# Kernel optimization log

Measured on AMD Instinct MI355X. Metric: run time of the kernel, lower is better.

Reference implementation:

```python
import jax, jax.numpy as jnp
import numpy as np

K_SIZE = 7
D_MODEL = 128
D_Q = 64
N_HEADS = 4
D_FF = 512
EPS = 1e-5


def _windows(x, k):
    # x: [N,E,H,W] -> [N,E,P,H,W]; zero-padded local k x k windows,
    # row-major over (dy,dx), matching nn.Unfold ordering.
    p = k // 2
    N, E, H, W = x.shape
    xp = jnp.pad(x, ((0, 0), (0, 0), (p, p), (p, p)))
    ws = [xp[:, :, i:i + H, j:j + W] for i in range(k) for j in range(k)]
    return jnp.stack(ws, axis=2)


def _layernorm(x, g, b):
    m = jnp.mean(x, -1, keepdims=True)
    v = jnp.var(x, -1, keepdims=True)
    return (x - m) * jax.lax.rsqrt(v + EPS) * g + b


def setup_inputs() -> dict:
    key = jax.random.key(0)
    ks = jax.random.split(key, 12)
    E, Q, F = D_MODEL, D_Q, D_FF

    def g(k, shape, s=0.02):
        return jax.random.normal(k, shape, jnp.float32) * s

    return dict(
        x=jax.random.normal(ks[0], (4, E, 64, 64), jnp.float32),
        qcoeff=jax.random.normal(ks[1], (4, Q), jnp.float32),
        wq=g(ks[2], (E, E)), bq=jnp.zeros((E,), jnp.float32),
        wk=g(ks[3], (E, E)), bk=jnp.zeros((E,), jnp.float32),
        wv=g(ks[4], (E, E)), bv=jnp.zeros((E,), jnp.float32),
        rel_bias=jnp.zeros((N_HEADS, K_SIZE * K_SIZE), jnp.float32),
        ln1_g=jnp.ones((E,), jnp.float32), ln1_b=jnp.zeros((E,), jnp.float32),
        bil_w=g(ks[5], (E, E, Q)), bil_b=jnp.zeros((E,), jnp.float32),
        ln2_g=jnp.ones((E,), jnp.float32), ln2_b=jnp.zeros((E,), jnp.float32),
        w1=g(ks[6], (F, E)), b1=jnp.zeros((F,), jnp.float32),
        w2=g(ks[7], (E, F)), b2=jnp.zeros((E,), jnp.float32),
    )


def reference(x, qcoeff, wq, bq, wk, bk, wv, bv, rel_bias, ln1_g, ln1_b,
              bil_w, bil_b, ln2_g, ln2_b, w1, b1, w2, b2):
    N, E, H, W = x.shape
    Nh = N_HEADS
    Hd = E // Nh
    P = K_SIZE * K_SIZE

    x_nhwc = jnp.transpose(x, (0, 2, 3, 1))              # [N,H,W,E]
    xn = _layernorm(x_nhwc, ln1_g, ln1_b)
    xnc = jnp.transpose(xn, (0, 3, 1, 2))                # [N,E,H,W]

    # 1x1-conv projections
    q = jnp.einsum('nchw,oc->nohw', xnc, wq) + bq[None, :, None, None]
    k = jnp.einsum('nchw,oc->nohw', xnc, wk) + bk[None, :, None, None]
    v = jnp.einsum('nchw,oc->nohw', xnc, wv) + bv[None, :, None, None]

    # local windows of K/V: [N,Nh,Hd,P,H,W]
    Kw = _windows(k, K_SIZE).reshape(N, Nh, Hd, P, H, W)
    Vw = _windows(v, K_SIZE).reshape(N, Nh, Hd, P, H, W)
    Qh = q.reshape(N, Nh, Hd, H, W)

    scores = jnp.einsum('nhdyx,nhdpyx->nhpyx', Qh, Kw)
    scores = scores + rel_bias[None, :, :, None, None]
    attn = jax.nn.softmax(scores, axis=2)                # softmax over P
    out = jnp.einsum('nhpyx,nhdpyx->nhdyx', attn, Vw).reshape(N, E, H, W)
    z0 = jnp.transpose(out, (0, 2, 3, 1))                # [N,H,W,E]

    # Bilinear(z0, qcoeff): qcoeff constant per (H,W) -> contract once per batch
    t = jnp.einsum('oiq,nq->noi', bil_w, qcoeff)         # [N,E,E]
    z1 = jnp.einsum('nhwi,noi->nhwo', z0, t) + bil_b

    z2 = z1 + x_nhwc
    z3 = _layernorm(z2, ln2_g, ln2_b)
    h1 = jax.nn.gelu(z3 @ w1.T + b1, approximate=False)  # dropout inactive (eval)
    z4 = h1 @ w2.T + b2 + z2
    return jnp.transpose(z4, (0, 3, 1, 2))               # [N,E,H,W]
```

## Files before the change

kernel.cpp:

```cpp
#include <hip/hip_runtime.h>
#include <cmath>

#define EPS 1e-5f
#define SZ 2097152

typedef __attribute__((ext_vector_type(8))) short short8;
typedef __attribute__((ext_vector_type(4))) float floatx4;

__device__ __forceinline__ float dot4(float4 a, float4 b) {
  return fmaf(a.x, b.x, fmaf(a.y, b.y, fmaf(a.z, b.z, a.w * b.w)));
}

__device__ __forceinline__ short f2bf(float f) {
  union { float f; unsigned u; } v; v.f = f;
  unsigned r = v.u + 0x7fff + ((v.u >> 16) & 1);
  return (short)(r >> 16);
}

#define MFMA16(a, b, c) __builtin_amdgcn_mfma_f32_16x16x32_bf16(a, b, c, 0, 0, 0)

__global__ __launch_bounds__(256) void k_prep(const float* __restrict__ w1,
    const float* __restrict__ w2, const float* __restrict__ wq,
    const float* __restrict__ wk, const float* __restrict__ wv,
    short* __restrict__ w1bf, short* __restrict__ w2bf,
    short* __restrict__ wqbf, short* __restrict__ wkbf, short* __restrict__ wvbf) {
  int tid0 = blockIdx.x * 256 + threadIdx.x;
  int stride = gridDim.x * 256;
  for (int i = tid0; i < 16384; i += stride) {
    int flat = i * 4; int f = flat >> 7, c = flat & 127;
    float4 v = *(const float4*)&w1[flat];
    short t4[4] = {f2bf(v.x), f2bf(v.y), f2bf(v.z), f2bf(v.w)};
    *(uint2*)&w1bf[f * 136 + c] = *(uint2*)t4;
  }
  for (int i = tid0; i < 16384; i += stride) {
    int flat = i * 4; int o = flat >> 9, j = flat & 511;
    int ck = j >> 7, jj = j & 127;
    float4 v = *(const float4*)&w2[flat];
    short t4[4] = {f2bf(v.x), f2bf(v.y), f2bf(v.z), f2bf(v.w)};
    *(uint2*)&w2bf[(ck * 128 + o) * 136 + jj] = *(uint2*)t4;
  }
  for (int i = tid0; i < 4096; i += stride) {
    int flat = i * 4; int o = flat >> 7, c = flat & 127;
    float4 a = *(const float4*)&wq[flat];
    float4 b = *(const float4*)&wk[flat];
    float4 cc = *(const float4*)&wv[flat];
    short ta[4] = {f2bf(a.x), f2bf(a.y), f2bf(a.z), f2bf(a.w)};
    short tb4[4] = {f2bf(b.x), f2bf(b.y), f2bf(b.z), f2bf(b.w)};
    short tc[4] = {f2bf(cc.x), f2bf(cc.y), f2bf(cc.z), f2bf(cc.w)};
    *(uint2*)&wqbf[o * 136 + c] = *(uint2*)ta;
    *(uint2*)&wkbf[o * 136 + c] = *(uint2*)tb4;
    *(uint2*)&wvbf[o * 136 + c] = *(uint2*)tc;
  }
}

__global__ __launch_bounds__(256) void k_ln1(const float* __restrict__ x,
    const float* __restrict__ g, const float* __restrict__ b,
    float* __restrict__ xnhwc, float* __restrict__ xn) {
  __shared__ float tile[128 * 65];
  __shared__ float mres[64], rres[64];
  int bid = blockIdx.x;
  int n = bid >> 6, y = bid & 63;
  const float* xb = x + (size_t)n * (128 * 64 * 64) + y * 64;
  int tid = threadIdx.x;
  for (int it = 0; it < 32; ++it) {
    int flat = it * 256 + tid;
    int c = flat >> 6, xp = flat & 63;
    tile[c * 65 + xp] = xb[(size_t)c * 4096 + xp];
  }
  __syncthreads();
  if (tid < 64) {
    float s = 0.f, sq = 0.f;
    for (int c = 0; c < 128; ++c) { float v = tile[c * 65 + tid]; s += v; sq += v * v; }
    float m = s * (1.f / 128.f);
    float var = sq * (1.f / 128.f) - m * m;
    mres[tid] = m;
    rres[tid] = rsqrtf(var + EPS);
  }
  __syncthreads();
  size_t rowbase = (size_t)bid * (64 * 128);
  for (int it = 0; it < 32; ++it) {
    int flat = it * 256 + tid;
    int c = flat & 127, px = flat >> 7;
    float v = tile[c * 65 + px];
    xnhwc[rowbase + flat] = v;
    xn[rowbase + flat] = (v - mres[px]) * rres[px] * g[c] + b[c];
  }
}

__global__ __launch_bounds__(1024) void k_qkv(const float* __restrict__ xn,
    const short* __restrict__ wqbf, const short* __restrict__ wkbf,
    const short* __restrict__ wvbf, const float* __restrict__ bq,
    const float* __restrict__ bk, const float* __restrict__ bv,
    short* __restrict__ qbf, short* __restrict__ kbf, short* __restrict__ vtb) {
  __shared__ __align__(16) short xs[64 * 136];
  __shared__ __align__(16) short ws[128 * 136];
  int tid = threadIdx.x;
  int bid = blockIdx.x;
  int n = bid >> 6, y = bid & 63;
  size_t rowbase = (size_t)bid * (64 * 128);
  for (int it = 0; it < 2; ++it) {
    int flat = (it * 1024 + tid) * 4;
    int px = flat >> 7, c = flat & 127;
    float4 xv = *(const float4*)&xn[rowbase + flat];
    short tmp[4] = {f2bf(xv.x), f2bf(xv.y), f2bf(xv.z), f2bf(xv.w)};
    *(uint2*)&xs[px * 136 + c] = *(uint2*)tmp;
  }
  __syncthreads();
  int w = tid >> 6, lane = tid & 63;
  int quad = lane >> 4, r16 = lane & 15;
  int wm = w & 3, wn = w >> 2;
  int strip = wm * 16;
  short8 a[4];
#pragma unroll
  for (int kk = 0; kk < 4; ++kk)
    a[kk] = *(const short8*)&xs[(strip + r16) * 136 + kk * 32 + quad * 8];
  const short* wptr[3] = {wqbf, wkbf, wvbf};
  const float* bptr[3] = {bq, bk, bv};
  for (int m = 0; m < 3; ++m) {
    __syncthreads();
    const short* wp = wptr[m];
    for (int i = tid; i < 2176; i += 1024)
      *(short8*)&ws[i * 8] = *(const short8*)&wp[i * 8];
    __syncthreads();
    const float* bb = bptr[m];
#pragma unroll
    for (int nt = 0; nt < 2; ++nt) {
      int o0 = wn * 32 + nt * 16;
      floatx4 acc = {0.f, 0.f, 0.f, 0.f};
#pragma unroll
      for (int kk = 0; kk < 4; ++kk) {
        short8 bfr = *(const short8*)&ws[(o0 + r16) * 136 + kk * 32 + quad * 8];
        acc = MFMA16(a[kk], bfr, acc);
      }
      float bv2 = bb[o0 + r16];
      if (m < 2) {
        short* dst = (m == 0) ? qbf : kbf;
        size_t base = (size_t)bid * 8192;
#pragma unroll
        for (int r = 0; r < 4; ++r) {
          int px = strip + quad * 4 + r;
          dst[base + px * 128 + o0 + r16] = f2bf(acc[r] + bv2);
        }
      } else {
        short t4[4] = {f2bf(acc[0] + bv2), f2bf(acc[1] + bv2),
                       f2bf(acc[2] + bv2), f2bf(acc[3] + bv2)};
        *(uint2*)&vtb[(size_t)(n * 128 + o0 + r16) * 4096 + y * 64 + strip + quad * 4] =
            *(uint2*)t4;
      }
    }
  }
}

__global__ __launch_bounds__(256) void k_attn(const short* __restrict__ qbf,
    const short* __restrict__ kbf, const short* __restrict__ vtb,
    const float* __restrict__ rel_bias, float* __restrict__ z0) {
  __shared__ __align__(16) char smem[44800 + 13312 + 9216 + 256];
  short* KV = (short*)smem;
  float* ssf = (float*)(smem + 44800);
  short* AbB = (short*)(smem + 44800 + 13312);
  float* bias = (float*)(smem + 44800 + 13312 + 9216);

  int bid = blockIdx.x;
  int h = bid & 3, y = (bid >> 2) & 63, n = bid >> 8;
  int tid = threadIdx.x;
  int w = tid >> 6, lane = tid & 63;
  int quad = lane >> 4, r16 = lane & 15;
  int strip = w * 16;
  short* Abw = AbB + w * (16 * 72);

  {
    unsigned* ad = (unsigned*)Abw;
    for (int i = lane; i < 576; i += 64) ad[i] = 0u;
  }
  short8 qf = *(const short8*)&qbf[(size_t)n * 524288 +
                                   (size_t)(y * 64 + strip + r16) * 128 + h * 32 + quad * 8];
  const short* kbp = kbf + (size_t)n * 524288 + h * 32;
  for (int u = tid; u < 1792; u += 256) {
    int r = u >> 8, rest = u & 255;
    int gx = rest >> 2, d8 = rest & 3;
    int yy = y + r - 3;
    if ((unsigned)yy < 64u) {
      uint4 v = *(const uint4*)&kbp[(size_t)(yy * 64 + gx) * 128 + d8 * 8];
      *(uint4*)&KV[(r * 80 + gx + 3) * 40 + d8 * 8] = v;
    }
  }
  if (tid < 49) bias[tid] = rel_bias[h * 49 + tid];
  __syncthreads();

  bool yyok[7];
#pragma unroll
  for (int r = 0; r < 7; ++r) yyok[r] = (unsigned)(y + r - 3) < 64u;
#pragma unroll
  for (int r = 0; r < 7; ++r) {
#pragma unroll
    for (int t = 0; t < 2; ++t) {
      int xxc = (w + t) * 16 + r16;
      short8 bf = *(const short8*)&KV[(r * 80 + xxc) * 40 + quad * 8];
      floatx4 c = MFMA16(qf, bf, ((floatx4){0.f, 0.f, 0.f, 0.f}));
#pragma unroll
      for (int rr = 0; rr < 4; ++rr) {
        int px = strip + quad * 4 + rr;
        int dx = xxc - px;
        if ((unsigned)dx < 7u) {
          int gxv = xxc - 3;
          float val = (yyok[r] && (unsigned)gxv < 64u) ? c[rr] : 0.f;
          ssf[px * 52 + r * 7 + dx] = val + bias[r * 7 + dx];
        }
      }
    }
  }
  __syncthreads();
  const short* vbp = vtb + (size_t)(n * 128 + h * 32) * 4096;
  for (int u = tid; u < 1792; u += 256) {
    int r = u >> 8, rest = u & 255;
    int d = rest >> 3, g = rest & 7;
    int yy = y + r - 3;
    uint4 v = {0u, 0u, 0u, 0u};
    if ((unsigned)yy < 64u)
      v = *(const uint4*)&vbp[(size_t)d * 4096 + yy * 64 + g * 8];
    *(uint4*)&KV[(r * 32 + d) * 72 + g * 8] = v;
  }
  {
    int px = tid >> 2, sub = tid & 3;
    int p0 = sub * 12, cnt = (sub == 3) ? 13 : 12;
    float sv[13];
    float mx = -1e30f;
    for (int pi = 0; pi < cnt; ++pi) { sv[pi] = ssf[px * 52 + p0 + pi]; mx = fmaxf(mx, sv[pi]); }
    mx = fmaxf(mx, __shfl_xor(mx, 1));
    mx = fmaxf(mx, __shfl_xor(mx, 2));
    float sum = 0.f;
    for (int pi = 0; pi < cnt; ++pi) { float e = __expf(sv[pi] - mx); sv[pi] = e; sum += e; }
    sum += __shfl_xor(sum, 1);
    sum += __shfl_xor(sum, 2);
    float inv = 1.f / sum;
    for (int pi = 0; pi < cnt; ++pi) ssf[px * 52 + p0 + pi] = sv[pi] * inv;
  }
  __syncthreads();
  floatx4 oacc[2] = {(floatx4){0.f, 0.f, 0.f, 0.f}, (floatx4){0.f, 0.f, 0.f, 0.f}};
  int lrow = lane >> 2, sub = lane & 3;
  int pxg = strip + lrow;
  int kk0 = (w == 3) ? 1 : 0;
  int kk1 = (w == 0) ? 0 : 1;
  for (int r = 0; r < 7; ++r) {
    int c0 = pxg + sub - 3;
    if ((unsigned)c0 < 64u) Abw[lrow * 72 + c0] = f2bf(ssf[pxg * 52 + r * 7 + sub]);
    int c1 = pxg + sub + 1;
    if (sub < 3 && (unsigned)c1 < 64u)
      Abw[lrow * 72 + c1] = f2bf(ssf[pxg * 52 + r * 7 + sub + 4]);
    for (int kk = kk0; kk <= kk1; ++kk) {
      short8 af = *(const short8*)&Abw[r16 * 72 + kk * 32 + quad * 8];
#pragma unroll
      for (int nt = 0; nt < 2; ++nt) {
        short8 vf = *(const short8*)&KV[(r * 32 + nt * 16 + r16) * 72 + kk * 32 + quad * 8];
        oacc[nt] = MFMA16(af, vf, oacc[nt]);
      }
    }
  }
  float* zrow = z0 + (size_t)n * 524288 + (size_t)y * 64 * 128 + h * 32;
#pragma unroll
  for (int nt = 0; nt < 2; ++nt)
#pragma unroll
    for (int rr = 0; rr < 4; ++rr) {
      int px = strip + quad * 4 + rr;
      zrow[px * 128 + nt * 16 + r16] = oacc[nt][rr];
    }
}

__global__ __launch_bounds__(256) void k_t(const float* __restrict__ bil_w,
    const float* __restrict__ qcoeff, short* __restrict__ t) {
  __shared__ float qs[4 * 64];
  int tid = threadIdx.x;
  qs[tid] = qcoeff[tid];
  __syncthreads();
  int flat = blockIdx.x * 256 + tid;
  const float* wrow = bil_w + (size_t)flat * 64;
  float acc[4] = {0.f, 0.f, 0.f, 0.f};
  for (int qq = 0; qq < 64; qq += 4) {
    float4 w4 = *(const float4*)&wrow[qq];
#pragma unroll
    for (int nn = 0; nn < 4; ++nn) {
      const float* qc = &qs[nn * 64 + qq];
      acc[nn] = fmaf(w4.x, qc[0], fmaf(w4.y, qc[1], fmaf(w4.z, qc[2], fmaf(w4.w, qc[3], acc[nn]))));
    }
  }
  int o = flat >> 7, i = flat & 127;
#pragma unroll
  for (int nn = 0; nn < 4; ++nn) t[nn * 17408 + o * 136 + i] = f2bf(acc[nn]);
}

__global__ __launch_bounds__(1024) void k_bil(const float* __restrict__ z0,
    const short* __restrict__ tb, const float* __restrict__ bil_b,
    const float* __restrict__ xnhwc, const float* __restrict__ g2,
    const float* __restrict__ b2ln, float* __restrict__ z2,
    float* __restrict__ z3) {
  __shared__ __align__(16) short zs[64 * 136];
  __shared__ __align__(16) short ts[128 * 136];
  __shared__ __align__(16) float z2s[64 * 132];
  int tid = threadIdx.x;
  int bid = blockIdx.x;
  int n = bid >> 6;
  size_t rowbase = (size_t)bid * (64 * 128);
  for (int it = 0; it < 2; ++it) {
    int flat = (it * 1024 + tid) * 4;
    int px = flat >> 7, c = flat & 127;
    float4 v = *(const float4*)&z0[rowbase + flat];
    short tmp[4] = {f2bf(v.x), f2bf(v.y), f2bf(v.z), f2bf(v.w)};
    *(uint2*)&zs[px * 136 + c] = *(uint2*)tmp;
  }
  const short* tn = tb + (size_t)n * 17408;
  for (int i = tid; i < 2176; i += 1024)
    *(short8*)&ts[i * 8] = *(const short8*)&tn[i * 8];
  __syncthreads();
  int w = tid >> 6, lane = tid & 63;
  int quad = lane >> 4, r16 = lane & 15;
  int wm = w & 3, wn = w >> 2;
  int strip = wm * 16;
  short8 a[4];
#pragma unroll
  for (int kk = 0; kk < 4; ++kk)
    a[kk] = *(const short8*)&zs[(strip + r16) * 136 + kk * 32 + quad * 8];
#pragma unroll
  for (int nt = 0; nt < 2; ++nt) {
    int o0 = wn * 32 + nt * 16;
    floatx4 acc = {0.f, 0.f, 0.f, 0.f};
#pragma unroll
    for (int kk = 0; kk < 4; ++kk) {
      short8 bfr = *(const short8*)&ts[(o0 + r16) * 136 + kk * 32 + quad * 8];
      acc = MFMA16(a[kk], bfr, acc);
    }
    float bb = bil_b[o0 + r16];
#pragma unroll
    for (int r = 0; r < 4; ++r) {
      int px = strip + quad * 4 + r;
      z2s[px * 132 + o0 + r16] = acc[r] + bb + xnhwc[rowbase + px * 128 + o0 + r16];
    }
  }
  __syncthreads();
  {
    int px = tid >> 4, cl = tid & 15;
    float4 v0 = *(const float4*)&z2s[px * 132 + cl * 8];
    float4 v1 = *(const float4*)&z2s[px * 132 + cl * 8 + 4];
    float s = v0.x + v0.y + v0.z + v0.w + v1.x + v1.y + v1.z + v1.w;
    float sq = dot4(v0, v0) + dot4(v1, v1);
    s += __shfl_xor(s, 1);  sq += __shfl_xor(sq, 1);
    s += __shfl_xor(s, 2);  sq += __shfl_xor(sq, 2);
    s += __shfl_xor(s, 4);  sq += __shfl_xor(sq, 4);
    s += __shfl_xor(s, 8);  sq += __shfl_xor(sq, 8);
    float m = s * (1.f / 128.f);
    float var = sq * (1.f / 128.f) - m * m;
    float rr = rsqrtf(var + EPS);
    int c0 = cl * 8;
    float o0v[8];
#pragma unroll
    for (int j = 0; j < 8; ++j) o0v[j] = (j < 4) ? (&v0.x)[j] : (&v1.x)[j - 4];
    float* z2p = &z2[rowbase + px * 128 + c0];
    float* z3p = &z3[rowbase + px * 128 + c0];
#pragma unroll
    for (int j = 0; j < 8; ++j) {
      z2p[j] = o0v[j];
      z3p[j] = (o0v[j] - m) * rr * g2[c0 + j] + b2ln[c0 + j];
    }
  }
}

__global__ __launch_bounds__(1024) void k_ffn(const float* __restrict__ z3,
    const float* __restrict__ z2, const short* __restrict__ w1bf,
    const float* __restrict__ b1, const short* __restrict__ w2bf,
    const float* __restrict__ b2, float* __restrict__ out) {
  __shared__ __align__(16) char smem[17408 + 34816 + 17408 + 34816];
  short* z3s = (short*)smem;
  short* w1c = (short*)(smem + 17408);
  short* h1s = (short*)(smem + 17408 + 34816);
  short* w2c = (short*)(smem + 17408 + 34816 + 17408);
  float* outt = (float*)(smem + 17408);
  int tid = threadIdx.x;
  int bid = blockIdx.x;
  int n = bid >> 6, y = bid & 63;
  size_t rowbase = (size_t)bid * (64 * 128);
  for (int it = 0; it < 2; ++it) {
    int flat = (it * 1024 + tid) * 4;
    int px = flat >> 7, c = flat & 127;
    float4 v = *(const float4*)&z3[rowbase + flat];
    short tmp[4] = {f2bf(v.x), f2bf(v.y), f2bf(v.z), f2bf(v.w)};
    *(uint2*)&z3s[px * 136 + c] = *(uint2*)tmp;
  }
  __syncthreads();
  int w = tid >> 6, lane = tid & 63;
  int quad = lane >> 4, r16 = lane & 15;
  int wm = w & 3, wn = w >> 2;
  int strip = wm * 16;
  short8 a3[4];
#pragma unroll
  for (int kk = 0; kk < 4; ++kk)
    a3[kk] = *(const short8*)&z3s[(strip + r16) * 136 + kk * 32 + quad * 8];
  floatx4 zacc[2];
  zacc[0] = (floatx4){0.f, 0.f, 0.f, 0.f};
  zacc[1] = (floatx4){0.f, 0.f, 0.f, 0.f};
  for (int fc = 0; fc < 512; fc += 128) {
    __syncthreads();
    const short* w1src = w1bf + fc * 136;
    const short* w2src = w2bf + (fc >> 7) * 17408;
    for (int i = tid; i < 2176; i += 1024) {
      *(short8*)&w1c[i * 8] = *(const short8*)&w1src[i * 8];
      *(short8*)&w2c[i * 8] = *(const short8*)&w2src[i * 8];
    }
    __syncthreads();
#pragma unroll
    for (int nt = 0; nt < 2; ++nt) {
      int f0 = wn * 32 + nt * 16;
      floatx4 acc = {0.f, 0.f, 0.f, 0.f};
#pragma unroll
      for (int kk = 0; kk < 4; ++kk) {
        short8 bfr = *(const short8*)&w1c[(f0 + r16) * 136 + kk * 32 + quad * 8];
        acc = MFMA16(a3[kk], bfr, acc);
      }
      float bb1 = b1[fc + f0 + r16];
#pragma unroll
      for (int r = 0; r < 4; ++r) {
        float hv = acc[r] + bb1;
        float ge = 0.5f * hv * (1.f + erff(hv * 0.70710678118f));
        h1s[(strip + quad * 4 + r) * 136 + f0 + r16] = f2bf(ge);
      }
    }
    __syncthreads();
    short8 ah[4];
#pragma unroll
    for (int kk = 0; kk < 4; ++kk)
      ah[kk] = *(const short8*)&h1s[(strip + r16) * 136 + kk * 32 + quad * 8];
#pragma unroll
    for (int nt = 0; nt < 2; ++nt) {
      int o0 = wn * 32 + nt * 16;
#pragma unroll
      for (int kk = 0; kk < 4; ++kk) {
        short8 bfr = *(const short8*)&w2c[(o0 + r16) * 136 + kk * 32 + quad * 8];
        zacc[nt] = MFMA16(ah[kk], bfr, zacc[nt]);
      }
    }
  }
  __syncthreads();
#pragma unroll
  for (int nt = 0; nt < 2; ++nt) {
    int o0 = wn * 32 + nt * 16;
    float bb = b2[o0 + r16];
#pragma unroll
    for (int r = 0; r < 4; ++r) {
      int px = strip + quad * 4 + r;
      outt[(o0 + r16) * 65 + px] =
          zacc[nt][r] + bb + z2[rowbase + px * 128 + o0 + r16];
    }
  }
  __syncthreads();
  for (int it = 0; it < 8; ++it) {
    int flat = it * 1024 + tid;
    int o = flat >> 6, px = flat & 63;
    out[(((size_t)(n * 128 + o)) * 64 + y) * 64 + px] = outt[o * 65 + px];
  }
}

extern "C" void kernel_launch(void* const* d_in, const int* in_sizes, int n_in,
                              void* d_out, int out_size, void* d_ws, size_t ws_size,
                              hipStream_t stream) {
  const float* x        = (const float*)d_in[0];
  const float* qcoeff   = (const float*)d_in[1];
  const float* wq       = (const float*)d_in[2];
  const float* bq       = (const float*)d_in[3];
  const float* wk       = (const float*)d_in[4];
  const float* bk       = (const float*)d_in[5];
  const float* wv       = (const float*)d_in[6];
  const float* bv       = (const float*)d_in[7];
  const float* rel_bias = (const float*)d_in[8];
  const float* ln1_g    = (const float*)d_in[9];
  const float* ln1_b    = (const float*)d_in[10];
  const float* bil_w    = (const float*)d_in[11];
  const float* bil_b    = (const float*)d_in[12];
  const float* ln2_g    = (const float*)d_in[13];
  const float* ln2_b    = (const float*)d_in[14];
  const float* w1       = (const float*)d_in[15];
  const float* b1       = (const float*)d_in[16];
  const float* w2       = (const float*)d_in[17];
  const float* b2       = (const float*)d_in[18];
  float* out = (float*)d_out;

  float* ws = (float*)d_ws;
  float* x_nhwc = ws;
  float* xn     = ws + 1 * SZ;
  short* qbf = (short*)(ws + 2 * SZ);
  short* kbf = qbf + SZ;
  short* vtb = kbf + SZ;
  float* z2 = ws + 2 * SZ;
  float* z3 = ws + 3 * SZ;
  short* bf     = (short*)(ws + 4 * SZ);
  short* tb     = bf;
  short* w1bf   = bf + 4 * 17408;
  short* w2bf   = w1bf + 512 * 136;
  short* wqbf   = w2bf + 4 * 17408;
  short* wkbf   = wqbf + 17408;
  short* wvbf   = wkbf + 17408;
  float* z0 = xn;

  k_prep<<<64, 256, 0, stream>>>(w1, w2, wq, wk, wv, w1bf, w2bf, wqbf, wkbf, wvbf);
  k_ln1<<<256, 256, 0, stream>>>(x, ln1_g, ln1_b, x_nhwc, xn);
  k_qkv<<<256, 1024, 0, stream>>>(xn, wqbf, wkbf, wvbf, bq, bk, bv, qbf, kbf, vtb);
  k_t<<<64, 256, 0, stream>>>(bil_w, qcoeff, tb);
  k_attn<<<1024, 256, 0, stream>>>(qbf, kbf, vtb, rel_bias, z0);
  k_bil<<<256, 1024, 0, stream>>>(z0, tb, bil_b, x_nhwc, ln2_g, ln2_b, z2, z3);
  k_ffn<<<256, 1024, 0, stream>>>(z3, z2, w1bf, b1, w2bf, b2, out);
}
```

Before: 174.3 us.

## Fuse kernels: prep+bilinear table, LN1+QKV, bilinear+LN2+FFN; attention reads global directly

Merges the bilinear-table computation into the weight prep kernel, fuses LayerNorm1 into the QKV projection, and fuses the bilinear, LayerNorm2 and FFN stages into a single tail kernel that keeps z2/z3 in shared memory. This cuts the kernel count from seven to four and removes the fp32 round trips of xn, z2 and z3 through global memory. The attention kernel drops its shared K/V staging and block-wide barriers, so each wave now loads K and V fragments straight from global memory. That trades shared-memory reuse for fewer syncs and higher occupancy, at the cost of redundant global and cache reads.

```diff
diff --git a/kernel.cpp b/kernel.cpp
--- a/kernel.cpp
+++ b/kernel.cpp
@@ -22,9 +22,15 @@
 __global__ __launch_bounds__(256) void k_prep(const float* __restrict__ w1,
     const float* __restrict__ w2, const float* __restrict__ wq,
     const float* __restrict__ wk, const float* __restrict__ wv,
+    const float* __restrict__ bil_w, const float* __restrict__ qcoeff,
     short* __restrict__ w1bf, short* __restrict__ w2bf,
-    short* __restrict__ wqbf, short* __restrict__ wkbf, short* __restrict__ wvbf) {
-  int tid0 = blockIdx.x * 256 + threadIdx.x;
+    short* __restrict__ wqbf, short* __restrict__ wkbf, short* __restrict__ wvbf,
+    short* __restrict__ tb) {
+  __shared__ float qs[256];
+  int tid = threadIdx.x;
+  qs[tid] = qcoeff[tid];
+  __syncthreads();
+  int tid0 = blockIdx.x * 256 + tid;
   int stride = gridDim.x * 256;
   for (int i = tid0; i < 16384; i += stride) {
     int flat = i * 4; int f = flat >> 7, c = flat & 127;
@@ -51,59 +57,72 @@
     *(uint2*)&wkbf[o * 136 + c] = *(uint2*)tb4;
     *(uint2*)&wvbf[o * 136 + c] = *(uint2*)tc;
   }
-}
-
-__global__ __launch_bounds__(256) void k_ln1(const float* __restrict__ x,
+  {
+    int flat = tid0;
+    const float* wrow = bil_w + (size_t)flat * 64;
+    float acc[4] = {0.f, 0.f, 0.f, 0.f};
+    for (int qq = 0; qq < 64; qq += 4) {
+      float4 w4 = *(const float4*)&wrow[qq];
+#pragma unroll
+      for (int nn = 0; nn < 4; ++nn) {
+        const float* qc = &qs[nn * 64 + qq];
+        acc[nn] = fmaf(w4.x, qc[0], fmaf(w4.y, qc[1], fmaf(w4.z, qc[2], fmaf(w4.w, qc[3], acc[nn]))));
+      }
+    }
+    int o = flat >> 7, i = flat & 127;
+#pragma unroll
+    for (int nn = 0; nn < 4; ++nn) tb[nn * 17408 + o * 136 + i] = f2bf(acc[nn]);
+  }
+}
+
+__global__ __launch_bounds__(1024) void k_qkvln(const float* __restrict__ x,
     const float* __restrict__ g, const float* __restrict__ b,
-    float* __restrict__ xnhwc, float* __restrict__ xn) {
-  __shared__ float tile[128 * 65];
-  __shared__ float mres[64], rres[64];
-  int bid = blockIdx.x;
-  int n = bid >> 6, y = bid & 63;
-  const float* xb = x + (size_t)n * (128 * 64 * 64) + y * 64;
-  int tid = threadIdx.x;
-  for (int it = 0; it < 32; ++it) {
-    int flat = it * 256 + tid;
-    int c = flat >> 6, xp = flat & 63;
-    tile[c * 65 + xp] = xb[(size_t)c * 4096 + xp];
-  }
-  __syncthreads();
-  if (tid < 64) {
-    float s = 0.f, sq = 0.f;
-    for (int c = 0; c < 128; ++c) { float v = tile[c * 65 + tid]; s += v; sq += v * v; }
-    float m = s * (1.f / 128.f);
-    float var = sq * (1.f / 128.f) - m * m;
-    mres[tid] = m;
-    rres[tid] = rsqrtf(var + EPS);
-  }
-  __syncthreads();
-  size_t rowbase = (size_t)bid * (64 * 128);
-  for (int it = 0; it < 32; ++it) {
-    int flat = it * 256 + tid;
-    int c = flat & 127, px = flat >> 7;
-    float v = tile[c * 65 + px];
-    xnhwc[rowbase + flat] = v;
-    xn[rowbase + flat] = (v - mres[px]) * rres[px] * g[c] + b[c];
-  }
-}
-
-__global__ __launch_bounds__(1024) void k_qkv(const float* __restrict__ xn,
     const short* __restrict__ wqbf, const short* __restrict__ wkbf,
     const short* __restrict__ wvbf, const float* __restrict__ bq,
     const float* __restrict__ bk, const float* __restrict__ bv,
-    short* __restrict__ qbf, short* __restrict__ kbf, short* __restrict__ vtb) {
+    float* __restrict__ xnhwc, short* __restrict__ qbf,
+    short* __restrict__ kbf, short* __restrict__ vtb) {
+  __shared__ float tile[128 * 65];
+  __shared__ float mres[64], rres[64];
   __shared__ __align__(16) short xs[64 * 136];
   __shared__ __align__(16) short ws[128 * 136];
   int tid = threadIdx.x;
   int bid = blockIdx.x;
   int n = bid >> 6, y = bid & 63;
-  size_t rowbase = (size_t)bid * (64 * 128);
-  for (int it = 0; it < 2; ++it) {
-    int flat = (it * 1024 + tid) * 4;
-    int px = flat >> 7, c = flat & 127;
-    float4 xv = *(const float4*)&xn[rowbase + flat];
-    short tmp[4] = {f2bf(xv.x), f2bf(xv.y), f2bf(xv.z), f2bf(xv.w)};
-    *(uint2*)&xs[px * 136 + c] = *(uint2*)tmp;
+  const float* xb = x + (size_t)n * (128 * 4096) + y * 64;
+  for (int it = 0; it < 8; ++it) {
+    int flat = it * 1024 + tid;
+    int c = flat >> 6, xp = flat & 63;
+    tile[c * 65 + xp] = xb[(size_t)c * 4096 + xp];
+  }
+  __syncthreads();
+  {
+    int px = tid >> 4, cl = tid & 15;
+    float s = 0.f, sq = 0.f;
+#pragma unroll
+    for (int j = 0; j < 8; ++j) {
+      float v = tile[(cl * 8 + j) * 65 + px];
+      s += v; sq += v * v;
+    }
+    s += __shfl_xor(s, 1);  sq += __shfl_xor(sq, 1);
+    s += __shfl_xor(s, 2);  sq += __shfl_xor(sq, 2);
+    s += __shfl_xor(s, 4);  sq += __shfl_xor(sq, 4);
+    s += __shfl_xor(s, 8);  sq += __shfl_xor(sq, 8);
+    if (cl == 0) {
+      float m = s * (1.f / 128.f);
+      float var = sq * (1.f / 128.f) - m * m;
+      mres[px] = m;
+      rres[px] = rsqrtf(var + EPS);
+    }
+  }
+  __syncthreads();
+  size_t rowbase = (size_t)bid * 8192;
+  for (int it = 0; it < 8; ++it) {
+    int flat = it * 1024 + tid;
+    int c = flat & 127, px = flat >> 7;
+    float v = tile[c * 65 + px];
+    xnhwc[rowbase + flat] = v;
+    xs[px * 136 + c] = f2bf((v - mres[px]) * rres[px] * g[c] + b[c]);
   }
   __syncthreads();
   int w = tid >> 6, lane = tid & 63;
@@ -135,11 +154,10 @@
       float bv2 = bb[o0 + r16];
       if (m < 2) {
         short* dst = (m == 0) ? qbf : kbf;
-        size_t base = (size_t)bid * 8192;
 #pragma unroll
         for (int r = 0; r < 4; ++r) {
           int px = strip + quad * 4 + r;
-          dst[base + px * 128 + o0 + r16] = f2bf(acc[r] + bv2);
+          dst[rowbase + px * 128 + o0 + r16] = f2bf(acc[r] + bv2);
         }
       } else {
         short t4[4] = {f2bf(acc[0] + bv2), f2bf(acc[1] + bv2),
@@ -154,78 +172,56 @@
 __global__ __launch_bounds__(256) void k_attn(const short* __restrict__ qbf,
     const short* __restrict__ kbf, const short* __restrict__ vtb,
     const float* __restrict__ rel_bias, float* __restrict__ z0) {
-  __shared__ __align__(16) char smem[44800 + 13312 + 9216 + 256];
-  short* KV = (short*)smem;
-  float* ssf = (float*)(smem + 44800);
-  short* AbB = (short*)(smem + 44800 + 13312);
-  float* bias = (float*)(smem + 44800 + 13312 + 9216);
-
+  __shared__ float ssf[4][16 * 50];
+  __shared__ __align__(16) short AbB[4][16 * 68];
+  __shared__ float biasS[4][52];
   int bid = blockIdx.x;
   int h = bid & 3, y = (bid >> 2) & 63, n = bid >> 8;
   int tid = threadIdx.x;
   int w = tid >> 6, lane = tid & 63;
   int quad = lane >> 4, r16 = lane & 15;
   int strip = w * 16;
-  short* Abw = AbB + w * (16 * 72);
-
+  float* ssfw = ssf[w];
+  short* Abw = AbB[w];
+  float* biasw = biasS[w];
   {
     unsigned* ad = (unsigned*)Abw;
-    for (int i = lane; i < 576; i += 64) ad[i] = 0u;
-  }
-  short8 qf = *(const short8*)&qbf[(size_t)n * 524288 +
-                                   (size_t)(y * 64 + strip + r16) * 128 + h * 32 + quad * 8];
+    for (int i = lane; i < 544; i += 64) ad[i] = 0u;
+  }
+  if (lane < 49) biasw[lane] = rel_bias[h * 49 + lane];
+  const short* qrow = qbf + (size_t)n * 524288 + (size_t)y * 64 * 128 + h * 32;
+  short8 qf = *(const short8*)&qrow[(strip + r16) * 128 + quad * 8];
   const short* kbp = kbf + (size_t)n * 524288 + h * 32;
-  for (int u = tid; u < 1792; u += 256) {
-    int r = u >> 8, rest = u & 255;
-    int gx = rest >> 2, d8 = rest & 3;
+#pragma unroll
+  for (int r = 0; r < 7; ++r) {
     int yy = y + r - 3;
-    if ((unsigned)yy < 64u) {
-      uint4 v = *(const uint4*)&kbp[(size_t)(yy * 64 + gx) * 128 + d8 * 8];
-      *(uint4*)&KV[(r * 80 + gx + 3) * 40 + d8 * 8] = v;
-    }
-  }
-  if (tid < 49) bias[tid] = rel_bias[h * 49 + tid];
-  __syncthreads();
-
-  bool yyok[7];
-#pragma unroll
-  for (int r = 0; r < 7; ++r) yyok[r] = (unsigned)(y + r - 3) < 64u;
-#pragma unroll
-  for (int r = 0; r < 7; ++r) {
+    bool yok = (unsigned)yy < 64u;
+    int yyc = min(max(yy, 0), 63);
 #pragma unroll
     for (int t = 0; t < 2; ++t) {
       int xxc = (w + t) * 16 + r16;
-      short8 bf = *(const short8*)&KV[(r * 80 + xxc) * 40 + quad * 8];
+      int gx = xxc - 3;
+      bool ok = yok && ((unsigned)gx < 64u);
+      int gxc = min(max(gx, 0), 63);
+      short8 bf = *(const short8*)&kbp[(size_t)(yyc * 64 + gxc) * 128 + quad * 8];
       floatx4 c = MFMA16(qf, bf, ((floatx4){0.f, 0.f, 0.f, 0.f}));
 #pragma unroll
       for (int rr = 0; rr < 4; ++rr) {
-        int px = strip + quad * 4 + rr;
-        int dx = xxc - px;
+        int lrow = quad * 4 + rr;
+        int dx = xxc - (strip + lrow);
         if ((unsigned)dx < 7u) {
-          int gxv = xxc - 3;
-          float val = (yyok[r] && (unsigned)gxv < 64u) ? c[rr] : 0.f;
-          ssf[px * 52 + r * 7 + dx] = val + bias[r * 7 + dx];
+          float val = ok ? c[rr] : 0.f;
+          ssfw[lrow * 50 + r * 7 + dx] = val + biasw[r * 7 + dx];
         }
       }
     }
   }
-  __syncthreads();
-  const short* vbp = vtb + (size_t)(n * 128 + h * 32) * 4096;
-  for (int u = tid; u < 1792; u += 256) {
-    int r = u >> 8, rest = u & 255;
-    int d = rest >> 3, g = rest & 7;
-    int yy = y + r - 3;
-    uint4 v = {0u, 0u, 0u, 0u};
-    if ((unsigned)yy < 64u)
-      v = *(const uint4*)&vbp[(size_t)d * 4096 + yy * 64 + g * 8];
-    *(uint4*)&KV[(r * 32 + d) * 72 + g * 8] = v;
-  }
-  {
-    int px = tid >> 2, sub = tid & 3;
+  {
+    int lrow = lane >> 2, sub = lane & 3;
     int p0 = sub * 12, cnt = (sub == 3) ? 13 : 12;
     float sv[13];
     float mx = -1e30f;
-    for (int pi = 0; pi < cnt; ++pi) { sv[pi] = ssf[px * 52 + p0 + pi]; mx = fmaxf(mx, sv[pi]); }
+    for (int pi = 0; pi < cnt; ++pi) { sv[pi] = ssfw[lrow * 50 + p0 + pi]; mx = fmaxf(mx, sv[pi]); }
     mx = fmaxf(mx, __shfl_xor(mx, 1));
     mx = fmaxf(mx, __shfl_xor(mx, 2));
     float sum = 0.f;
@@ -233,25 +229,29 @@
     sum += __shfl_xor(sum, 1);
     sum += __shfl_xor(sum, 2);
     float inv = 1.f / sum;
-    for (int pi = 0; pi < cnt; ++pi) ssf[px * 52 + p0 + pi] = sv[pi] * inv;
-  }
-  __syncthreads();
+    for (int pi = 0; pi < cnt; ++pi) ssfw[lrow * 50 + p0 + pi] = sv[pi] * inv;
+  }
   floatx4 oacc[2] = {(floatx4){0.f, 0.f, 0.f, 0.f}, (floatx4){0.f, 0.f, 0.f, 0.f}};
+  int kk0 = (w == 3) ? 1 : 0;
+  int kk1 = (w == 0) ? 0 : 1;
   int lrow = lane >> 2, sub = lane & 3;
   int pxg = strip + lrow;
-  int kk0 = (w == 3) ? 1 : 0;
-  int kk1 = (w == 0) ? 0 : 1;
+  const short* vbp = vtb + (size_t)(n * 128 + h * 32) * 4096;
   for (int r = 0; r < 7; ++r) {
+    int yy = y + r - 3;
+    bool yok = (unsigned)yy < 64u;
+    int yyc = min(max(yy, 0), 63);
     int c0 = pxg + sub - 3;
-    if ((unsigned)c0 < 64u) Abw[lrow * 72 + c0] = f2bf(ssf[pxg * 52 + r * 7 + sub]);
+    if ((unsigned)c0 < 64u) Abw[lrow * 68 + c0] = f2bf(ssfw[lrow * 50 + r * 7 + sub]);
     int c1 = pxg + sub + 1;
     if (sub < 3 && (unsigned)c1 < 64u)
-      Abw[lrow * 72 + c1] = f2bf(ssf[pxg * 52 + r * 7 + sub + 4]);
+      Abw[lrow * 68 + c1] = f2bf(ssfw[lrow * 50 + r * 7 + sub + 4]);
     for (int kk = kk0; kk <= kk1; ++kk) {
-      short8 af = *(const short8*)&Abw[r16 * 72 + kk * 32 + quad * 8];
+      short8 af = *(const short8*)&Abw[r16 * 68 + kk * 32 + quad * 8];
 #pragma unroll
       for (int nt = 0; nt < 2; ++nt) {
-        short8 vf = *(const short8*)&KV[(r * 32 + nt * 16 + r16) * 72 + kk * 32 + quad * 8];
+        short8 vf = *(const short8*)&vbp[(size_t)(nt * 16 + r16) * 4096 + yyc * 64 + kk * 32 + quad * 8];
+        if (!yok) vf = (short8){0, 0, 0, 0, 0, 0, 0, 0};
         oacc[nt] = MFMA16(af, vf, oacc[nt]);
       }
     }
@@ -266,73 +266,58 @@
     }
 }
 
-__global__ __launch_bounds__(256) void k_t(const float* __restrict__ bil_w,
-    const float* __restrict__ qcoeff, short* __restrict__ t) {
-  __shared__ float qs[4 * 64];
-  int tid = threadIdx.x;
-  qs[tid] = qcoeff[tid];
-  __syncthreads();
-  int flat = blockIdx.x * 256 + tid;
-  const float* wrow = bil_w + (size_t)flat * 64;
-  float acc[4] = {0.f, 0.f, 0.f, 0.f};
-  for (int qq = 0; qq < 64; qq += 4) {
-    float4 w4 = *(const float4*)&wrow[qq];
-#pragma unroll
-    for (int nn = 0; nn < 4; ++nn) {
-      const float* qc = &qs[nn * 64 + qq];
-      acc[nn] = fmaf(w4.x, qc[0], fmaf(w4.y, qc[1], fmaf(w4.z, qc[2], fmaf(w4.w, qc[3], acc[nn]))));
-    }
-  }
-  int o = flat >> 7, i = flat & 127;
-#pragma unroll
-  for (int nn = 0; nn < 4; ++nn) t[nn * 17408 + o * 136 + i] = f2bf(acc[nn]);
-}
-
-__global__ __launch_bounds__(1024) void k_bil(const float* __restrict__ z0,
+__global__ __launch_bounds__(1024) void k_tail(const float* __restrict__ z0,
     const short* __restrict__ tb, const float* __restrict__ bil_b,
     const float* __restrict__ xnhwc, const float* __restrict__ g2,
-    const float* __restrict__ b2ln, float* __restrict__ z2,
-    float* __restrict__ z3) {
-  __shared__ __align__(16) short zs[64 * 136];
-  __shared__ __align__(16) short ts[128 * 136];
-  __shared__ __align__(16) float z2s[64 * 132];
+    const float* __restrict__ b2ln, const short* __restrict__ w1bf,
+    const float* __restrict__ b1, const short* __restrict__ w2bf,
+    const float* __restrict__ b2, float* __restrict__ out) {
+  __shared__ __align__(16) char smem[34816 + 34816 + 17408 + 17408 + 33792];
+  short* R1s = (short*)smem;
+  short* w2c = (short*)(smem + 34816);
+  short* z3s = (short*)(smem + 69632);
+  short* h1s = (short*)(smem + 87040);
+  float* z2s = (float*)(smem + 104448);
+  float* outt = (float*)smem;
   int tid = threadIdx.x;
   int bid = blockIdx.x;
-  int n = bid >> 6;
-  size_t rowbase = (size_t)bid * (64 * 128);
+  int n = bid >> 6, y = bid & 63;
+  size_t rowbase = (size_t)bid * 8192;
   for (int it = 0; it < 2; ++it) {
     int flat = (it * 1024 + tid) * 4;
     int px = flat >> 7, c = flat & 127;
     float4 v = *(const float4*)&z0[rowbase + flat];
     short tmp[4] = {f2bf(v.x), f2bf(v.y), f2bf(v.z), f2bf(v.w)};
-    *(uint2*)&zs[px * 136 + c] = *(uint2*)tmp;
+    *(uint2*)&z3s[px * 136 + c] = *(uint2*)tmp;
   }
   const short* tn = tb + (size_t)n * 17408;
   for (int i = tid; i < 2176; i += 1024)
-    *(short8*)&ts[i * 8] = *(const short8*)&tn[i * 8];
+    *(short8*)&R1s[i * 8] = *(const short8*)&tn[i * 8];
   __syncthreads();
   int w = tid >> 6, lane = tid & 63;
   int quad = lane >> 4, r16 = lane & 15;
   int wm = w & 3, wn = w >> 2;
   int strip = wm * 16;
-  short8 a[4];
-#pragma unroll
-  for (int kk = 0; kk < 4; ++kk)
-    a[kk] = *(const short8*)&zs[(strip + r16) * 136 + kk * 32 + quad * 8];
-#pragma unroll
-  for (int nt = 0; nt < 2; ++nt) {
-    int o0 = wn * 32 + nt * 16;
-    floatx4 acc = {0.f, 0.f, 0.f, 0.f};
-#pragma unroll
-    for (int kk = 0; kk < 4; ++kk) {
-      short8 bfr = *(const short8*)&ts[(o0 + r16) * 136 + kk * 32 + quad * 8];
-      acc = MFMA16(a[kk], bfr, acc);
-    }
-    float bb = bil_b[o0 + r16];
-#pragma unroll
-    for (int r = 0; r < 4; ++r) {
-      int px = strip + quad * 4 + r;
-      z2s[px * 132 + o0 + r16] = acc[r] + bb + xnhwc[rowbase + px * 128 + o0 + r16];
+  {
+    short8 a[4];
+#pragma unroll
+    for (int kk = 0; kk < 4; ++kk)
+      a[kk] = *(const short8*)&z3s[(strip + r16) * 136 + kk * 32 + quad * 8];
+#pragma unroll
+    for (int nt = 0; nt < 2; ++nt) {
+      int o0 = wn * 32 + nt * 16;
+      floatx4 acc = {0.f, 0.f, 0.f, 0.f};
+#pragma unroll
+      for (int kk = 0; kk < 4; ++kk) {
+        short8 bfr = *(const short8*)&R1s[(o0 + r16) * 136 + kk * 32 + quad * 8];
+        acc = MFMA16(a[kk], bfr, acc);
+      }
+      float bb = bil_b[o0 + r16];
+#pragma unroll
+      for (int r = 0; r < 4; ++r) {
+        int px = strip + quad * 4 + r;
+        z2s[px * 132 + o0 + r16] = acc[r] + bb + xnhwc[rowbase + px * 128 + o0 + r16];
+      }
     }
   }
   __syncthreads();
@@ -350,45 +335,15 @@
     float var = sq * (1.f / 128.f) - m * m;
     float rr = rsqrtf(var + EPS);
     int c0 = cl * 8;
-    float o0v[8];
-#pragma unroll
-    for (int j = 0; j < 8; ++j) o0v[j] = (j < 4) ? (&v0.x)[j] : (&v1.x)[j - 4];
-    float* z2p = &z2[rowbase + px * 128 + c0];
-    float* z3p = &z3[rowbase + px * 128 + c0];
+    short t8[8];
 #pragma unroll
     for (int j = 0; j < 8; ++j) {
-      z2p[j] = o0v[j];
-      z3p[j] = (o0v[j] - m) * rr * g2[c0 + j] + b2ln[c0 + j];
-    }
-  }
-}
-
-__global__ __launch_bounds__(1024) void k_ffn(const float* __restrict__ z3,
-    const float* __restrict__ z2, const short* __restrict__ w1bf,
-    const float* __restrict__ b1, const short* __restrict__ w2bf,
-    const float* __restrict__ b2, float* __restrict__ out) {
-  __shared__ __align__(16) char smem[17408 + 34816 + 17408 + 34816];
-  short* z3s = (short*)smem;
-  short* w1c = (short*)(smem + 17408);
-  short* h1s = (short*)(smem + 17408 + 34816);
-  short* w2c = (short*)(smem + 17408 + 34816 + 17408);
-  float* outt = (float*)(smem + 17408);
-  int tid = threadIdx.x;
-  int bid = blockIdx.x;
-  int n = bid >> 6, y = bid & 63;
-  size_t rowbase = (size_t)bid * (64 * 128);
-  for (int it = 0; it < 2; ++it) {
-    int flat = (it * 1024 + tid) * 4;
-    int px = flat >> 7, c = flat & 127;
-    float4 v = *(const float4*)&z3[rowbase + flat];
-    short tmp[4] = {f2bf(v.x), f2bf(v.y), f2bf(v.z), f2bf(v.w)};
-    *(uint2*)&z3s[px * 136 + c] = *(uint2*)tmp;
-  }
-  __syncthreads();
-  int w = tid >> 6, lane = tid & 63;
-  int quad = lane >> 4, r16 = lane & 15;
-  int wm = w & 3, wn = w >> 2;
-  int strip = wm * 16;
+      float vv = (j < 4) ? (&v0.x)[j] : (&v1.x)[j - 4];
+      t8[j] = f2bf((vv - m) * rr * g2[c0 + j] + b2ln[c0 + j]);
+    }
+    *(uint4*)&z3s[px * 136 + c0] = *(uint4*)t8;
+  }
+  __syncthreads();
   short8 a3[4];
 #pragma unroll
   for (int kk = 0; kk < 4; ++kk)
@@ -401,7 +356,7 @@
     const short* w1src = w1bf + fc * 136;
     const short* w2src = w2bf + (fc >> 7) * 17408;
     for (int i = tid; i < 2176; i += 1024) {
-      *(short8*)&w1c[i * 8] = *(const short8*)&w1src[i * 8];
+      *(short8*)&R1s[i * 8] = *(const short8*)&w1src[i * 8];
       *(short8*)&w2c[i * 8] = *(const short8*)&w2src[i * 8];
     }
     __syncthreads();
@@ -411,7 +366,7 @@
       floatx4 acc = {0.f, 0.f, 0.f, 0.f};
 #pragma unroll
       for (int kk = 0; kk < 4; ++kk) {
-        short8 bfr = *(const short8*)&w1c[(f0 + r16) * 136 + kk * 32 + quad * 8];
+        short8 bfr = *(const short8*)&R1s[(f0 + r16) * 136 + kk * 32 + quad * 8];
         acc = MFMA16(a3[kk], bfr, acc);
       }
       float bb1 = b1[fc + f0 + r16];
@@ -445,8 +400,7 @@
 #pragma unroll
     for (int r = 0; r < 4; ++r) {
       int px = strip + quad * 4 + r;
-      outt[(o0 + r16) * 65 + px] =
-          zacc[nt][r] + bb + z2[rowbase + px * 128 + o0 + r16];
+      outt[(o0 + r16) * 65 + px] = zacc[nt][r] + bb + z2s[px * 132 + o0 + r16];
     }
   }
   __syncthreads();
@@ -483,12 +437,10 @@
 
   float* ws = (float*)d_ws;
   float* x_nhwc = ws;
-  float* xn     = ws + 1 * SZ;
+  float* z0     = ws + 1 * SZ;
   short* qbf = (short*)(ws + 2 * SZ);
   short* kbf = qbf + SZ;
   short* vtb = kbf + SZ;
-  float* z2 = ws + 2 * SZ;
-  float* z3 = ws + 3 * SZ;
   short* bf     = (short*)(ws + 4 * SZ);
   short* tb     = bf;
   short* w1bf   = bf + 4 * 17408;
@@ -496,13 +448,12 @@
   short* wqbf   = w2bf + 4 * 17408;
   short* wkbf   = wqbf + 17408;
   short* wvbf   = wkbf + 17408;
-  float* z0 = xn;
-
-  k_prep<<<64, 256, 0, stream>>>(w1, w2, wq, wk, wv, w1bf, w2bf, wqbf, wkbf, wvbf);
-  k_ln1<<<256, 256, 0, stream>>>(x, ln1_g, ln1_b, x_nhwc, xn);
-  k_qkv<<<256, 1024, 0, stream>>>(xn, wqbf, wkbf, wvbf, bq, bk, bv, qbf, kbf, vtb);
-  k_t<<<64, 256, 0, stream>>>(bil_w, qcoeff, tb);
+
+  k_prep<<<64, 256, 0, stream>>>(w1, w2, wq, wk, wv, bil_w, qcoeff,
+                                 w1bf, w2bf, wqbf, wkbf, wvbf, tb);
+  k_qkvln<<<256, 1024, 0, stream>>>(x, ln1_g, ln1_b, wqbf, wkbf, wvbf,
+                                    bq, bk, bv, x_nhwc, qbf, kbf, vtb);
   k_attn<<<1024, 256, 0, stream>>>(qbf, kbf, vtb, rel_bias, z0);
-  k_bil<<<256, 1024, 0, stream>>>(z0, tb, bil_b, x_nhwc, ln2_g, ln2_b, z2, z3);
-  k_ffn<<<256, 1024, 0, stream>>>(z3, z2, w1bf, b1, w2bf, b2, out);
-}
+  k_tail<<<256, 1024, 0, stream>>>(z0, tb, bil_b, x_nhwc, ln2_g, ln2_b,
+                                   w1bf, b1, w2bf, b2, out);
+}
```

Result: faster. 151.7 us (-13.0%).
